# Optimization experiments

Hardware: AMD Instinct MI355X
Metric: run time of the kernel (lower is better)

## Reference

```python
import jax, jax.numpy as jnp
import numpy as np

C_SKIP = 64       # channels of a and of b (concat -> 128)
C_OUT = 64
N = 131072        # coarse nodes
E = 1048576       # directed edges (avg degree 8)
N_FINE = 4 * N    # fine mesh nodes after unpool
K = 3 * N_FINE    # unpool scatter assignments


def setup_inputs() -> dict:
    key = jax.random.key(0)
    ks = jax.random.split(key, 9)
    return {
        "a": jax.random.normal(ks[0], (C_SKIP, N), dtype=jnp.float32),
        "b": jax.random.normal(ks[1], (C_SKIP, N), dtype=jnp.float32),
        "W_self": jax.random.normal(ks[2], (C_OUT, 2 * C_SKIP), dtype=jnp.float32) * 0.05,
        "W_neigh": jax.random.normal(ks[3], (C_OUT, 2 * C_SKIP), dtype=jnp.float32) * 0.05,
        "bias": jax.random.normal(ks[4], (C_OUT,), dtype=jnp.float32) * 0.05,
        "gather_index": jax.random.randint(ks[5], (E,), 0, N),
        "reduce_index": jax.random.randint(ks[6], (E,), 0, N),
        "unpool_src": jax.random.randint(ks[7], (K,), 0, N),
        "unpool_dst": jax.random.randint(ks[8], (K,), 0, N_FINE),
    }


def reference(a, b, W_self, W_neigh, bias, gather_index, reduce_index, unpool_src, unpool_dst):
    # concat skip connection along channel dim (-2)
    x = jnp.concatenate((a, b), axis=-2)                  # [C_in, N]
    n = x.shape[-1]
    # GraphConv: gather source features along edges, segment-sum into targets
    msgs = x[:, gather_index]                              # [C_in, E]
    agg = jax.ops.segment_sum(msgs.T, reduce_index, num_segments=n).T  # [C_in, N]
    h = W_self @ x + W_neigh @ agg + bias[:, None]         # [C_out, N]
    h = jax.nn.relu(h)
    # GraphUnpool with reduce='amax': scatter-max coarse features to fine mesh
    out = jnp.zeros((h.shape[0], 4 * n), dtype=h.dtype)
    out = out.at[:, unpool_dst].max(h[:, unpool_src])      # [C_out, N_fine]
    return out
```

## Files before the change

kernel.cpp:

```cpp
#include <hip/hip_runtime.h>
#include <stdint.h>

constexpr int NN = 131072;
constexpr int EE = 1048576;
constexpr int NF = 4 * NN;
constexpr int KK = 3 * NF;

constexpr int NBLK = 256;
constexpr int SH_E = 6;
constexpr int SH_K = 7;
constexpr int NB_E = NN >> SH_E;
constexpr int NB_K = NF >> SH_K;
constexpr int EPT_E = EE / NBLK / 256;
constexpr int EPT_K = KK / NBLK / 256;
constexpr int CAP_E = 2048;
constexpr int CAP_K = 1024;

typedef __attribute__((ext_vector_type(8))) short bf16x8;
typedef __attribute__((ext_vector_type(4))) float f32x4;

__device__ inline uint32_t bf16rn(float f) {
    uint32_t u = __float_as_uint(f);
    return (u + 0x7FFFu + ((u >> 16) & 1u)) >> 16;
}
__device__ inline uint32_t pack2(float lo, float hi) {
    return bf16rn(lo) | (bf16rn(hi) << 16);
}
__device__ inline float bf_lo(uint32_t v) { return __uint_as_float(v << 16); }
__device__ inline float bf_hi(uint32_t v) { return __uint_as_float(v & 0xFFFF0000u); }

__global__ __launch_bounds__(256) void k_transpose(
    const float* __restrict__ a, const float* __restrict__ b,
    uint32_t* __restrict__ xTb)
{
    __shared__ float tile[128][33];
    int i0 = blockIdx.x * 32;
    for (int f = threadIdx.x; f < 128 * 32; f += 256) {
        int c = f >> 5, j = f & 31;
        const float* src = (c < 64) ? a : b;
        tile[c][j] = src[(size_t)(c & 63) * NN + i0 + j];
    }
    __syncthreads();
    for (int f = threadIdx.x; f < 64 * 32; f += 256) {
        int p = f & 63, j = f >> 6;
        xTb[(size_t)(i0 + j) * 64 + p] = pack2(tile[2 * p][j], tile[2 * p + 1][j]);
    }
}

template<int NB, int EPT>
__global__ __launch_bounds__(256) void k_sortpass1(
    const int* __restrict__ idx, int shift, int* __restrict__ histG)
{
    __shared__ int hist[NB];
    for (int f = threadIdx.x; f < NB; f += 256) hist[f] = 0;
    __syncthreads();
    int base = blockIdx.x * (256 * EPT);
#pragma unroll
    for (int u = 0; u < EPT; ++u) {
        int b = idx[base + u * 256 + threadIdx.x] >> shift;
        atomicAdd(&hist[b], 1);
    }
    __syncthreads();
    for (int f = threadIdx.x; f < NB; f += 256)
        histG[f * NBLK + blockIdx.x] = hist[f];
}

__global__ __launch_bounds__(256) void k_scan_bsum(
    const int* __restrict__ cnt, int* __restrict__ bsum)
{
    __shared__ int s[256];
    int base = blockIdx.x * 2048;
    int sum = 0;
    for (int j = threadIdx.x; j < 2048; j += 256) sum += cnt[base + j];
    s[threadIdx.x] = sum;
    __syncthreads();
    for (int o = 128; o > 0; o >>= 1) {
        if (threadIdx.x < o) s[threadIdx.x] += s[threadIdx.x + o];
        __syncthreads();
    }
    if (threadIdx.x == 0) bsum[blockIdx.x] = s[0];
}

__global__ __launch_bounds__(512) void k_scan_exc(int* __restrict__ bsum, int nblk)
{
    __shared__ int s[512];
    int t = threadIdx.x;
    s[t] = (t < nblk) ? bsum[t] : 0;
    __syncthreads();
    for (int o = 1; o < 512; o <<= 1) {
        int v = (t >= o) ? s[t - o] : 0;
        __syncthreads();
        s[t] += v;
        __syncthreads();
    }
    if (t < nblk) bsum[t] = (t == 0) ? 0 : s[t - 1];
}

__global__ __launch_bounds__(256) void k_scan_final(
    int* __restrict__ offs, int nb, const int* __restrict__ bsum)
{
    __shared__ int ts[256];
    int base = blockIdx.x * 2048 + threadIdx.x * 8;
    int loc[8];
    int sum = 0;
#pragma unroll
    for (int u = 0; u < 8; ++u) {
        int v = offs[base + u];
        loc[u] = sum;
        sum += v;
    }
    ts[threadIdx.x] = sum;
    __syncthreads();
    for (int o = 1; o < 256; o <<= 1) {
        int v = (threadIdx.x >= o) ? ts[threadIdx.x - o] : 0;
        __syncthreads();
        ts[threadIdx.x] += v;
        __syncthreads();
    }
    int texc = (threadIdx.x == 0) ? 0 : ts[threadIdx.x - 1];
    int bb = bsum[blockIdx.x];
#pragma unroll
    for (int u = 0; u < 8; ++u) offs[base + u] = bb + texc + loc[u];
    if (blockIdx.x == gridDim.x - 1 && threadIdx.x == 255) offs[nb] = bb + ts[255];
}

template<int NB, int EPT>
__global__ __launch_bounds__(256) void k_sortpass2(
    const int* __restrict__ idx, const int* __restrict__ payload, int shift,
    const int* __restrict__ offsG, uint32_t* __restrict__ pairs)
{
    __shared__ int curs[NB];
    for (int f = threadIdx.x; f < NB; f += 256)
        curs[f] = offsG[f * NBLK + blockIdx.x];
    __syncthreads();
    int lmask = (1 << shift) - 1;
    int base = blockIdx.x * (256 * EPT);
#pragma unroll
    for (int u = 0; u < EPT; ++u) {
        int e = base + u * 256 + threadIdx.x;
        int bk = idx[e];
        int pos = atomicAdd(&curs[bk >> shift], 1);
        pairs[pos] = (uint32_t)payload[e] | ((uint32_t)(bk & lmask) << 17);
    }
}

__global__ __launch_bounds__(256) void k_aggcsr(
    const uint32_t* __restrict__ xTb, const int* __restrict__ offsE,
    const uint32_t* __restrict__ pairsE, uint32_t* __restrict__ aggB)
{
    __shared__ uint32_t list[CAP_E];
    __shared__ int offs[65];
    __shared__ int curs[64];
    __shared__ int cnt_s;
    int bin = blockIdx.x;
    if (threadIdx.x == 0) {
        int beg = offsE[bin * NBLK];
        cnt_s = min(offsE[(bin + 1) * NBLK] - beg, CAP_E);
    }
    if (threadIdx.x < 64) curs[threadIdx.x] = 0;
    __syncthreads();
    int beg = offsE[bin * NBLK];
    int cnt = cnt_s;
    for (int i = threadIdx.x; i < cnt; i += 256)
        atomicAdd(&curs[(pairsE[beg + i] >> 17) & 63], 1);
    __syncthreads();
    if (threadIdx.x == 0) {
        int run = 0;
        for (int j = 0; j < 64; ++j) {
            offs[j] = run;
            run += curs[j];
            curs[j] = offs[j];
        }
        offs[64] = run;
    }
    __syncthreads();
    for (int i = threadIdx.x; i < cnt; i += 256) {
        uint32_t u = pairsE[beg + i];
        int p = atomicAdd(&curs[(u >> 17) & 63], 1);
        list[p] = u;
    }
    __syncthreads();

    int w = threadIdx.x >> 6, lane = threadIdx.x & 63;
    int n0 = w * 16, n1 = n0 + 16;
    int e0 = offs[n0], e1 = offs[n1];
    size_t rowbase = (size_t)(bin * 64) * 64 + lane;
    float sx = 0.f, sy = 0.f;
    int cur = n0;
    for (int e = e0; e < e1; e += 8) {
        int nb = e1 - e;
        uint32_t pr[8], v[8];
#pragma unroll
        for (int j = 0; j < 8; ++j)
            pr[j] = list[e + ((j < nb) ? j : (nb - 1))];
#pragma unroll
        for (int j = 0; j < 8; ++j)
            v[j] = xTb[(size_t)(pr[j] & 0x1FFFF) * 64 + lane];
#pragma unroll
        for (int j = 0; j < 8; ++j) {
            if (j < nb) {
                int d = (pr[j] >> 17) & 63;
                if (d != cur) {
                    aggB[rowbase + (size_t)cur * 64] = pack2(sx, sy);
                    for (int z = cur + 1; z < d; ++z)
                        aggB[rowbase + (size_t)z * 64] = 0u;
                    cur = d;
                    sx = 0.f; sy = 0.f;
                }
                sx += bf_lo(v[j]);
                sy += bf_hi(v[j]);
            }
        }
    }
    aggB[rowbase + (size_t)cur * 64] = pack2(sx, sy);
    for (int z = cur + 1; z < n1; ++z)
        aggB[rowbase + (size_t)z * 64] = 0u;
}

__global__ __launch_bounds__(256) void k_gemm(
    const uint32_t* __restrict__ xTb, const uint32_t* __restrict__ aggB,
    const float* __restrict__ Wself, const float* __restrict__ Wneigh,
    const float* __restrict__ bias, uint32_t* __restrict__ hT)
{
    int lane = threadIdx.x & 63;
    int wid = blockIdx.x * 4 + (threadIdx.x >> 6);
    int lr = lane & 15, lq = lane >> 4;

    bf16x8 wf[4][8];
#pragma unroll
    for (int mt = 0; mt < 4; ++mt) {
#pragma unroll
        for (int kt = 0; kt < 8; ++kt) {
            const float* W = (kt < 4) ? Wself : Wneigh;
            const float* p = W + (size_t)(mt * 16 + lr) * 128 + (kt & 3) * 32 + lq * 8;
            bf16x8 v;
#pragma unroll
            for (int j = 0; j < 8; ++j) v[j] = (short)bf16rn(p[j]);
            wf[mt][kt] = v;
        }
    }
    float bv[4][4];
#pragma unroll
    for (int mt = 0; mt < 4; ++mt)
#pragma unroll
        for (int r = 0; r < 4; ++r)
            bv[mt][r] = bias[mt * 16 + lq * 4 + r];

    const int NG = NN / 16;
    int stride = gridDim.x * 4;
    for (int g = wid; g < NG; g += stride) {
        int n = g * 16 + lr;
        const uint32_t* xr = xTb + (size_t)n * 64 + lq * 4;
        const uint32_t* ar = aggB + (size_t)n * 64 + lq * 4;
        bf16x8 bq[8];
#pragma unroll
        for (int kt = 0; kt < 4; ++kt)
            bq[kt] = *reinterpret_cast<const bf16x8*>(xr + kt * 16);
#pragma unroll
        for (int kt = 0; kt < 4; ++kt)
            bq[4 + kt] = *reinterpret_cast<const bf16x8*>(ar + kt * 16);
#pragma unroll
        for (int mt = 0; mt < 4; ++mt) {
            f32x4 acc = {0.f, 0.f, 0.f, 0.f};
#pragma unroll
            for (int kt = 0; kt < 8; ++kt)
                acc = __builtin_amdgcn_mfma_f32_16x16x32_bf16(wf[mt][kt], bq[kt], acc, 0, 0, 0);
            uint32_t u0 = pack2(fmaxf(acc[0] + bv[mt][0], 0.f), fmaxf(acc[1] + bv[mt][1], 0.f));
            uint32_t u1 = pack2(fmaxf(acc[2] + bv[mt][2], 0.f), fmaxf(acc[3] + bv[mt][3], 0.f));
            *reinterpret_cast<uint2*>(hT + (size_t)n * 32 + mt * 8 + lq * 2) = make_uint2(u0, u1);
        }
    }
}

__global__ __launch_bounds__(256) void k_unpoolcsr(
    const uint16_t* __restrict__ hT16, const int* __restrict__ offsK,
    const uint32_t* __restrict__ pairsK, float* __restrict__ out)
{
    __shared__ uint32_t list[CAP_K];
    __shared__ int offs[129];
    __shared__ int curs[128];
    __shared__ uint16_t buf[128][65];
    __shared__ int cnt_s;
    int bin = blockIdx.x;
    if (threadIdx.x == 0) {
        int beg = offsK[bin * NBLK];
        cnt_s = min(offsK[(bin + 1) * NBLK] - beg, CAP_K);
    }
    if (threadIdx.x < 128) curs[threadIdx.x] = 0;
    for (int f = threadIdx.x; f < 128 * 65; f += 256) ((uint16_t*)buf)[f] = 0;
    __syncthreads();
    int beg = offsK[bin * NBLK];
    int cnt = cnt_s;
    for (int i = threadIdx.x; i < cnt; i += 256)
        atomicAdd(&curs[(pairsK[beg + i] >> 17) & 127], 1);
    __syncthreads();
    if (threadIdx.x == 0) {
        int run = 0;
        for (int j = 0; j < 128; ++j) {
            offs[j] = run;
            run += curs[j];
            curs[j] = offs[j];
        }
        offs[128] = run;
    }
    __syncthreads();
    for (int i = threadIdx.x; i < cnt; i += 256) {
        uint32_t u = pairsK[beg + i];
        int p = atomicAdd(&curs[(u >> 17) & 127], 1);
        list[p] = u;
    }
    __syncthreads();

    int w = threadIdx.x >> 6, lane = threadIdx.x & 63;
    int n0 = w * 32, n1 = n0 + 32;
    int e0 = offs[n0], e1 = offs[n1];
    uint32_t m = 0;
    int cur = n0;
    for (int e = e0; e < e1; e += 8) {
        int nb = e1 - e;
        uint32_t pr[8], v[8];
#pragma unroll
        for (int j = 0; j < 8; ++j)
            pr[j] = list[e + ((j < nb) ? j : (nb - 1))];
#pragma unroll
        for (int j = 0; j < 8; ++j)
            v[j] = hT16[(size_t)(pr[j] & 0x1FFFF) * 64 + lane];
#pragma unroll
        for (int j = 0; j < 8; ++j) {
            if (j < nb) {
                int d = (pr[j] >> 17) & 127;
                if (d != cur) {
                    buf[cur][lane] = (uint16_t)m;
                    cur = d;
                    m = 0;
                }
                m = max(m, v[j]);
            }
        }
    }
    buf[cur][lane] = (uint16_t)m;
    __syncthreads();
    int j0 = bin << 7;
    for (int f = threadIdx.x; f < 64 * 128; f += 256) {
        int c = f >> 7, j = f & 127;
        out[(size_t)c * NF + j0 + j] = __uint_as_float(((uint32_t)buf[j][c]) << 16);
    }
}

extern "C" void kernel_launch(void* const* d_in, const int* in_sizes, int n_in,
                              void* d_out, int out_size, void* d_ws, size_t ws_size,
                              hipStream_t stream)
{
    const float* a      = (const float*)d_in[0];
    const float* b      = (const float*)d_in[1];
    const float* Wself  = (const float*)d_in[2];
    const float* Wneigh = (const float*)d_in[3];
    const float* bias   = (const float*)d_in[4];
    const int* gather_i = (const int*)d_in[5];
    const int* reduce_i = (const int*)d_in[6];
    const int* up_src   = (const int*)d_in[7];
    const int* up_dst   = (const int*)d_in[8];
    float* out = (float*)d_out;

    uint32_t* xTb   = (uint32_t*)d_ws;
    uint32_t* aggB  = xTb + (size_t)NN * 64;
    uint32_t* hT    = aggB + (size_t)NN * 64;
    uint32_t* pairsK= hT + (size_t)NN * 32;
    int* offsE      = (int*)(pairsK + KK);
    int* offsK      = offsE + (size_t)NB_E * NBLK + 1;
    int* bsum       = offsK + (size_t)NB_K * NBLK + 1;
    uint32_t* pairsE= hT;

    size_t need = ((size_t)NN * 160 + KK +
                   (size_t)NB_E * NBLK + 1 + (size_t)NB_K * NBLK + 1 + 1024) * 4;
    if (ws_size < need) return;

    k_transpose<<<NN / 32, 256, 0, stream>>>(a, b, xTb);

    k_sortpass1<NB_E, EPT_E><<<NBLK, 256, 0, stream>>>(reduce_i, SH_E, offsE);
    k_scan_bsum<<<NB_E * NBLK / 2048, 256, 0, stream>>>(offsE, bsum);
    k_scan_exc<<<1, 512, 0, stream>>>(bsum, NB_E * NBLK / 2048);
    k_scan_final<<<NB_E * NBLK / 2048, 256, 0, stream>>>(offsE, NB_E * NBLK, bsum);
    k_sortpass2<NB_E, EPT_E><<<NBLK, 256, 0, stream>>>(reduce_i, gather_i, SH_E, offsE, pairsE);

    k_sortpass1<NB_K, EPT_K><<<NBLK, 256, 0, stream>>>(up_dst, SH_K, offsK);
    k_scan_bsum<<<NB_K * NBLK / 2048, 256, 0, stream>>>(offsK, bsum);
    k_scan_exc<<<1, 512, 0, stream>>>(bsum, NB_K * NBLK / 2048);
    k_scan_final<<<NB_K * NBLK / 2048, 256, 0, stream>>>(offsK, NB_K * NBLK, bsum);
    k_sortpass2<NB_K, EPT_K><<<NBLK, 256, 0, stream>>>(up_dst, up_src, SH_K, offsK, pairsK);

    k_aggcsr<<<NB_E, 256, 0, stream>>>(xTb, offsE, pairsE, aggB);

    k_gemm<<<512, 256, 0, stream>>>(xTb, aggB, Wself, Wneigh, bias, hT);

    k_unpoolcsr<<<NB_K, 256, 0, stream>>>((const uint16_t*)hT, offsK, pairsK, out);
}
```

Measured before the change: 295.5 us.

## Merge the two bucket sorts into shared launches and deepen gather unroll

The edge and unpool counting sorts now run in single combined launches: one histogram kernel, one shared prefix scan over both histograms, and one scatter kernel. The separate exclusive-scan kernel is dropped, because each final-scan block now sums the preceding block totals itself. Ten sort launches become four, which cuts launch gaps and lets the two sorts fill the GPU together. The gather loops in the aggregation and unpool kernels also go from 8 to 16 outstanding loads, adding memory-level parallelism at the cost of more registers.

Result: faster. 264.3 us (-10.6%).

```diff
diff --git a/kernel.cpp b/kernel.cpp
--- a/kernel.cpp
+++ b/kernel.cpp
@@ -15,6 +15,9 @@
 constexpr int EPT_K = KK / NBLK / 256;
 constexpr int CAP_E = 2048;
 constexpr int CAP_K = 1024;
+constexpr int KOFF = NB_E * NBLK;
+constexpr int NH   = NB_E * NBLK + NB_K * NBLK;
+constexpr int NSCB = NH / 2048;
 
 typedef __attribute__((ext_vector_type(8))) short bf16x8;
 typedef __attribute__((ext_vector_type(4))) float f32x4;
@@ -48,13 +51,12 @@
 }
 
 template<int NB, int EPT>
-__global__ __launch_bounds__(256) void k_sortpass1(
-    const int* __restrict__ idx, int shift, int* __restrict__ histG)
-{
-    __shared__ int hist[NB];
+__device__ void pass1_body(const int* __restrict__ idx, int shift,
+                           int* __restrict__ histG, int blk, int* hist)
+{
     for (int f = threadIdx.x; f < NB; f += 256) hist[f] = 0;
     __syncthreads();
-    int base = blockIdx.x * (256 * EPT);
+    int base = blk * (256 * EPT);
 #pragma unroll
     for (int u = 0; u < EPT; ++u) {
         int b = idx[base + u * 256 + threadIdx.x] >> shift;
@@ -62,10 +64,21 @@
     }
     __syncthreads();
     for (int f = threadIdx.x; f < NB; f += 256)
-        histG[f * NBLK + blockIdx.x] = hist[f];
-}
-
-__global__ __launch_bounds__(256) void k_scan_bsum(
+        histG[f * NBLK + blk] = hist[f];
+}
+
+__global__ __launch_bounds__(256) void k_pass1(
+    const int* __restrict__ reduce_i, const int* __restrict__ up_dst,
+    int* __restrict__ histG)
+{
+    __shared__ int hist[NB_K];
+    if (blockIdx.x < NBLK)
+        pass1_body<NB_E, EPT_E>(reduce_i, SH_E, histG, blockIdx.x, hist);
+    else
+        pass1_body<NB_K, EPT_K>(up_dst, SH_K, histG + KOFF, blockIdx.x - NBLK, hist);
+}
+
+__global__ __launch_bounds__(256) void k_bsum(
     const int* __restrict__ cnt, int* __restrict__ bsum)
 {
     __shared__ int s[256];
@@ -81,25 +94,21 @@
     if (threadIdx.x == 0) bsum[blockIdx.x] = s[0];
 }
 
-__global__ __launch_bounds__(512) void k_scan_exc(int* __restrict__ bsum, int nblk)
-{
-    __shared__ int s[512];
-    int t = threadIdx.x;
-    s[t] = (t < nblk) ? bsum[t] : 0;
-    __syncthreads();
-    for (int o = 1; o < 512; o <<= 1) {
-        int v = (t >= o) ? s[t - o] : 0;
+__global__ __launch_bounds__(256) void k_final(
+    int* __restrict__ offs, const int* __restrict__ bsum)
+{
+    __shared__ int ts[256];
+    int partial = 0;
+    for (int i = threadIdx.x; i < blockIdx.x; i += 256) partial += bsum[i];
+    ts[threadIdx.x] = partial;
+    __syncthreads();
+    for (int o = 128; o > 0; o >>= 1) {
+        if (threadIdx.x < o) ts[threadIdx.x] += ts[threadIdx.x + o];
         __syncthreads();
-        s[t] += v;
-        __syncthreads();
-    }
-    if (t < nblk) bsum[t] = (t == 0) ? 0 : s[t - 1];
-}
-
-__global__ __launch_bounds__(256) void k_scan_final(
-    int* __restrict__ offs, int nb, const int* __restrict__ bsum)
-{
-    __shared__ int ts[256];
+    }
+    int bb = ts[0];
+    __syncthreads();
+
     int base = blockIdx.x * 2048 + threadIdx.x * 8;
     int loc[8];
     int sum = 0;
@@ -118,23 +127,22 @@
         __syncthreads();
     }
     int texc = (threadIdx.x == 0) ? 0 : ts[threadIdx.x - 1];
-    int bb = bsum[blockIdx.x];
 #pragma unroll
     for (int u = 0; u < 8; ++u) offs[base + u] = bb + texc + loc[u];
-    if (blockIdx.x == gridDim.x - 1 && threadIdx.x == 255) offs[nb] = bb + ts[255];
+    if (blockIdx.x == gridDim.x - 1 && threadIdx.x == 255) offs[NH] = bb + ts[255];
 }
 
 template<int NB, int EPT>
-__global__ __launch_bounds__(256) void k_sortpass2(
-    const int* __restrict__ idx, const int* __restrict__ payload, int shift,
-    const int* __restrict__ offsG, uint32_t* __restrict__ pairs)
-{
-    __shared__ int curs[NB];
+__device__ void pass2_body(const int* __restrict__ idx,
+                           const int* __restrict__ payload, int shift,
+                           const int* __restrict__ offsG, int sub,
+                           uint32_t* __restrict__ pairs, int blk, int* curs)
+{
     for (int f = threadIdx.x; f < NB; f += 256)
-        curs[f] = offsG[f * NBLK + blockIdx.x];
+        curs[f] = offsG[f * NBLK + blk] - sub;
     __syncthreads();
     int lmask = (1 << shift) - 1;
-    int base = blockIdx.x * (256 * EPT);
+    int base = blk * (256 * EPT);
 #pragma unroll
     for (int u = 0; u < EPT; ++u) {
         int e = base + u * 256 + threadIdx.x;
@@ -142,6 +150,21 @@
         int pos = atomicAdd(&curs[bk >> shift], 1);
         pairs[pos] = (uint32_t)payload[e] | ((uint32_t)(bk & lmask) << 17);
     }
+}
+
+__global__ __launch_bounds__(256) void k_pass2(
+    const int* __restrict__ reduce_i, const int* __restrict__ gather_i,
+    const int* __restrict__ up_dst, const int* __restrict__ up_src,
+    const int* __restrict__ offs,
+    uint32_t* __restrict__ pairsE, uint32_t* __restrict__ pairsK)
+{
+    __shared__ int curs[NB_K];
+    if (blockIdx.x < NBLK)
+        pass2_body<NB_E, EPT_E>(reduce_i, gather_i, SH_E, offs, 0,
+                                pairsE, blockIdx.x, curs);
+    else
+        pass2_body<NB_K, EPT_K>(up_dst, up_src, SH_K, offs + KOFF, EE,
+                                pairsK, blockIdx.x - NBLK, curs);
 }
 
 __global__ __launch_bounds__(256) void k_aggcsr(
@@ -187,17 +210,17 @@
     size_t rowbase = (size_t)(bin * 64) * 64 + lane;
     float sx = 0.f, sy = 0.f;
     int cur = n0;
-    for (int e = e0; e < e1; e += 8) {
+    for (int e = e0; e < e1; e += 16) {
         int nb = e1 - e;
-        uint32_t pr[8], v[8];
-#pragma unroll
-        for (int j = 0; j < 8; ++j)
+        uint32_t pr[16], v[16];
+#pragma unroll
+        for (int j = 0; j < 16; ++j)
             pr[j] = list[e + ((j < nb) ? j : (nb - 1))];
 #pragma unroll
-        for (int j = 0; j < 8; ++j)
+        for (int j = 0; j < 16; ++j)
             v[j] = xTb[(size_t)(pr[j] & 0x1FFFF) * 64 + lane];
 #pragma unroll
-        for (int j = 0; j < 8; ++j) {
+        for (int j = 0; j < 16; ++j) {
             if (j < nb) {
                 int d = (pr[j] >> 17) & 63;
                 if (d != cur) {
@@ -283,13 +306,13 @@
     __shared__ int cnt_s;
     int bin = blockIdx.x;
     if (threadIdx.x == 0) {
-        int beg = offsK[bin * NBLK];
-        cnt_s = min(offsK[(bin + 1) * NBLK] - beg, CAP_K);
+        int beg = offsK[bin * NBLK] - EE;
+        cnt_s = min(offsK[(bin + 1) * NBLK] - EE - beg, CAP_K);
     }
     if (threadIdx.x < 128) curs[threadIdx.x] = 0;
     for (int f = threadIdx.x; f < 128 * 65; f += 256) ((uint16_t*)buf)[f] = 0;
     __syncthreads();
-    int beg = offsK[bin * NBLK];
+    int beg = offsK[bin * NBLK] - EE;
     int cnt = cnt_s;
     for (int i = threadIdx.x; i < cnt; i += 256)
         atomicAdd(&curs[(pairsK[beg + i] >> 17) & 127], 1);
@@ -316,17 +339,17 @@
     int e0 = offs[n0], e1 = offs[n1];
     uint32_t m = 0;
     int cur = n0;
-    for (int e = e0; e < e1; e += 8) {
+    for (int e = e0; e < e1; e += 16) {
         int nb = e1 - e;
-        uint32_t pr[8], v[8];
-#pragma unroll
-        for (int j = 0; j < 8; ++j)
+        uint32_t pr[16], v[16];
+#pragma unroll
+        for (int j = 0; j < 16; ++j)
             pr[j] = list[e + ((j < nb) ? j : (nb - 1))];
 #pragma unroll
-        for (int j = 0; j < 8; ++j)
+        for (int j = 0; j < 16; ++j)
             v[j] = hT16[(size_t)(pr[j] & 0x1FFFF) * 64 + lane];
 #pragma unroll
-        for (int j = 0; j < 8; ++j) {
+        for (int j = 0; j < 16; ++j) {
             if (j < nb) {
                 int d = (pr[j] >> 17) & 127;
                 if (d != cur) {
@@ -366,32 +389,25 @@
     uint32_t* aggB  = xTb + (size_t)NN * 64;
     uint32_t* hT    = aggB + (size_t)NN * 64;
     uint32_t* pairsK= hT + (size_t)NN * 32;
-    int* offsE      = (int*)(pairsK + KK);
-    int* offsK      = offsE + (size_t)NB_E * NBLK + 1;
-    int* bsum       = offsK + (size_t)NB_K * NBLK + 1;
+    int* offs       = (int*)(pairsK + KK);
+    int* bsum       = offs + (size_t)NH + 1;
     uint32_t* pairsE= hT;
 
-    size_t need = ((size_t)NN * 160 + KK +
-                   (size_t)NB_E * NBLK + 1 + (size_t)NB_K * NBLK + 1 + 1024) * 4;
+    size_t need = ((size_t)NN * 160 + KK + (size_t)NH + 1 + NSCB) * 4;
     if (ws_size < need) return;
 
     k_transpose<<<NN / 32, 256, 0, stream>>>(a, b, xTb);
 
-    k_sortpass1<NB_E, EPT_E><<<NBLK, 256, 0, stream>>>(reduce_i, SH_E, offsE);
-    k_scan_bsum<<<NB_E * NBLK / 2048, 256, 0, stream>>>(offsE, bsum);
-    k_scan_exc<<<1, 512, 0, stream>>>(bsum, NB_E * NBLK / 2048);
-    k_scan_final<<<NB_E * NBLK / 2048, 256, 0, stream>>>(offsE, NB_E * NBLK, bsum);
-    k_sortpass2<NB_E, EPT_E><<<NBLK, 256, 0, stream>>>(reduce_i, gather_i, SH_E, offsE, pairsE);
-
-    k_sortpass1<NB_K, EPT_K><<<NBLK, 256, 0, stream>>>(up_dst, SH_K, offsK);
-    k_scan_bsum<<<NB_K * NBLK / 2048, 256, 0, stream>>>(offsK, bsum);
-    k_scan_exc<<<1, 512, 0, stream>>>(bsum, NB_K * NBLK / 2048);
-    k_scan_final<<<NB_K * NBLK / 2048, 256, 0, stream>>>(offsK, NB_K * NBLK, bsum);
-    k_sortpass2<NB_K, EPT_K><<<NBLK, 256, 0, stream>>>(up_dst, up_src, SH_K, offsK, pairsK);
-
-    k_aggcsr<<<NB_E, 256, 0, stream>>>(xTb, offsE, pairsE, aggB);
+    k_pass1<<<2 * NBLK, 256, 0, stream>>>(reduce_i, up_dst, offs);
+    k_bsum<<<NSCB, 256, 0, stream>>>(offs, bsum);
+    k_final<<<NSCB, 256, 0, stream>>>(offs, bsum);
+    k_pass2<<<2 * NBLK, 256, 0, stream>>>(reduce_i, gather_i, up_dst, up_src,
+                                          offs, pairsE, pairsK);
+
+    k_aggcsr<<<NB_E, 256, 0, stream>>>(xTb, offs, pairsE, aggB);
 
     k_gemm<<<512, 256, 0, stream>>>(xTb, aggB, Wself, Wneigh, bias, hT);
 
-    k_unpoolcsr<<<NB_K, 256, 0, stream>>>((const uint16_t*)hT, offsK, pairsK, out);
-}
+    k_unpoolcsr<<<NB_K, 256, 0, stream>>>((const uint16_t*)hT, offs + KOFF,
+                                          pairsK, out);
+}
```
